# Performance work log

Measured on AMD Instinct MI355X. Metric: run time of the kernel, lower is better.

Reference implementation:

```python
import jax, jax.numpy as jnp
import numpy as np

SIZE = 256.0           # network input resolution (source: SIZE = 256)
MAX_PER_CLASS = 50     # max_output_size_per_class
MAX_TOTAL = 50         # max_total_size
IOU_THR = 0.45
SCORE_THR = 0.4


def setup_inputs() -> dict:
    key = jax.random.key(0)
    k1, k2, k3 = jax.random.split(key, 3)
    B, N, C = 64, 4032, 80
    # pixel-scale centers and sizes, as produced by the YOLO head
    xy = jax.random.uniform(k1, (B, N, 2), minval=0.0, maxval=SIZE)
    wh = jax.random.uniform(k2, (B, N, 2), minval=4.0, maxval=96.0)
    box_xywh = jnp.concatenate([xy, wh], axis=-1)
    # squared uniform -> realistic sparsity of scores above 0.4 threshold
    scores = jax.random.uniform(k3, (B, N, C)) ** 2
    return {"box_xywh": box_xywh, "scores": scores}


def _decode(box_xywh):
    # xywh (pixels) -> normalized [y1, x1, y2, x2]  (filter_boxes math)
    box_yx = box_xywh[..., 1::-1]   # (x,y) -> (y,x)
    box_hw = box_xywh[..., 3:1:-1]  # (w,h) -> (h,w)
    mins = (box_yx - box_hw * 0.5) / SIZE
    maxes = (box_yx + box_hw * 0.5) / SIZE
    return jnp.concatenate([mins, maxes], axis=-1)


def _iou_one_to_many(box, boxes):
    # box [4], boxes [N,4], yxyx format
    yx1 = jnp.maximum(box[:2], boxes[:, :2])
    yx2 = jnp.minimum(box[2:], boxes[:, 2:])
    inter = jnp.prod(jnp.clip(yx2 - yx1, 0.0), axis=-1)
    a1 = jnp.prod(jnp.clip(box[2:] - box[:2], 0.0))
    a2 = jnp.prod(jnp.clip(boxes[:, 2:] - boxes[:, :2], 0.0), axis=-1)
    return inter / (a1 + a2 - inter + 1e-9)


def _nms_single_class(boxes, scores):
    # greedy NMS for one (batch, class) lane. boxes [N,4], scores [N]
    NEG = jnp.float32(-1.0)
    s0 = jnp.where(scores >= SCORE_THR, scores, NEG)  # score filtering (filter_boxes + NMS threshold)

    def body(s, _):
        i = jnp.argmax(s)
        best = s[i]
        valid = best > 0.0
        iou = _iou_one_to_many(boxes[i], boxes)
        suppress = (iou > IOU_THR) & valid
        s = jnp.where(suppress, NEG, s).at[i].set(NEG)
        return s, (i, jnp.where(valid, best, 0.0), valid)

    _, (idx, sel, valid) = jax.lax.scan(body, s0, None, length=MAX_PER_CLASS)
    return idx, sel, valid  # each [MAX_PER_CLASS]


def _combined_nms_one_image(boxes, scores):
    # boxes [N,4] shared across classes, scores [N,C]  (combined_non_max_suppression
    # with boxes reshaped to [B,N,1,4] -> class-agnostic box coordinates)
    C = scores.shape[1]
    idx, sel, valid = jax.vmap(lambda s: _nms_single_class(boxes, s))(scores.T)  # [C,50] each
    cls_ids = jnp.broadcast_to(jnp.arange(C)[:, None], idx.shape)
    flat_scores = jnp.where(valid, sel, -1.0).reshape(-1)   # [C*50]
    top_scores, top_i = jax.lax.top_k(flat_scores, MAX_TOTAL)
    box_idx = idx.reshape(-1)[top_i]
    keep = top_scores > 0.0
    out_boxes = jnp.clip(boxes[box_idx], 0.0, 1.0)          # clip_boxes=True default
    out_boxes = jnp.where(keep[:, None], out_boxes, 0.0)
    out_scores = jnp.where(keep, top_scores, 0.0)
    out_classes = jnp.where(keep, cls_ids.reshape(-1)[top_i].astype(jnp.float32), 0.0)
    n_valid = jnp.sum(keep).astype(jnp.int32)
    return out_boxes, out_scores, out_classes, n_valid


def reference(box_xywh, scores):
    boxes = _decode(box_xywh)  # [B,N,4] normalized yxyx
    out_boxes, out_scores, out_classes, valid_detections = jax.vmap(_combined_nms_one_image)(boxes, scores)
    return out_boxes, out_scores, out_classes, valid_detections
```

## Files before the change

### kernel.cpp

```cpp
#include <hip/hip_runtime.h>
#include <cstdint>
#include <cstddef>

#pragma clang fp contract(off)

#define B_IMG 64
#define N_BOX 4032
#define C_CLS 80
#define NCH 63
#define MAX_PER_CLASS 50
#define MAX_TOTAL 50
#define FCAP 512
#define T1 0.9216f
#define T2 0.81f

__device__ __constant__ float d_flo[6] = {T1, T2, 0.6724f, 0.5476f, 0.4356f, 0.4f};

__device__ __forceinline__ float bcastf(float v, int l) {
    return __uint_as_float((unsigned)__builtin_amdgcn_readlane((int)__float_as_uint(v), l));
}
__device__ __forceinline__ unsigned long long readlane64(unsigned long long v, int l) {
    unsigned lo = (unsigned)__builtin_amdgcn_readlane((int)(unsigned)v, l);
    unsigned hi = (unsigned)__builtin_amdgcn_readlane((int)(v >> 32), l);
    return ((unsigned long long)hi << 32) | lo;
}

__device__ __forceinline__ bool iou_sup(float ay0, float ax0, float ay1, float ax1, float a1,
                                        float by0, float bx0, float by1, float bx1, float a2) {
    float y1 = fmaxf(ay0, by0), x1 = fmaxf(ax0, bx0);
    float y2 = fminf(ay1, by1), x2 = fminf(ax1, bx1);
    float inter = fmaxf(y2 - y1, 0.f) * fmaxf(x2 - x1, 0.f);
    float denom = ((a1 + a2) - inter) + 1e-9f;
    float p = 0.45f * denom;
    float diff = inter - p;
    if (__builtin_fabsf(diff) <= 2e-6f * p) return (inter / denom) > 0.45f;
    return diff > 0.f;
}

__device__ __forceinline__ int nth_set(unsigned long long m, int r) {
    int src = 0, c;
    c = __popc((unsigned)m);
    if (r >= c) { src = 32; r -= c; m >>= 32; }
    unsigned mm = (unsigned)m;
    c = __popc(mm & 0xFFFFu); if (r >= c) { src += 16; r -= c; mm >>= 16; }
    c = __popc(mm & 0xFFu);   if (r >= c) { src += 8;  r -= c; mm >>= 8; }
    c = __popc(mm & 0xFu);    if (r >= c) { src += 4;  r -= c; mm >>= 4; }
    c = __popc(mm & 0x3u);    if (r >= c) { src += 2;  r -= c; mm >>= 2; }
    c = __popc(mm & 0x1u);    if (r >= c) { src += 1; }
    return src;
}

template <int NR>
__device__ __forceinline__ void sort_buf(unsigned long long* buf, int count, int lane) {
    unsigned long long lk[NR];
    int rk[NR];
#pragma unroll
    for (int r = 0; r < NR; ++r) {
        int slot = r * 64 + lane;
        lk[r] = (slot < count) ? buf[slot] : 0ull;
        rk[r] = 0;
    }
    __builtin_amdgcn_wave_barrier();
    for (int j = 0; j < count; ++j) {
        unsigned long long kj = buf[j];
#pragma unroll
        for (int r = 0; r < NR; ++r) rk[r] += (lk[r] < kj) ? 1 : 0;
    }
    __builtin_amdgcn_wave_barrier();
#pragma unroll
    for (int r = 0; r < NR; ++r) {
        int slot = r * 64 + lane;
        if (slot < count) buf[rk[r]] = lk[r];
    }
    __builtin_amdgcn_wave_barrier();
}

__global__ __launch_bounds__(256) void fused_decode_filter(const float4* __restrict__ xywh,
                                                           const float4* __restrict__ s4,
                                                           float4* __restrict__ obox,
                                                           unsigned long long* __restrict__ bm1,
                                                           unsigned long long* __restrict__ bm2) {
    const int tid = blockIdx.x * 256 + threadIdx.x;
    const int lane = threadIdx.x & 63;
    {
        float4 v = xywh[tid];
        float hh = v.w * 0.5f, hw = v.z * 0.5f;
        float4 o;
        o.x = (v.y - hh) * (1.0f / 256.0f);
        o.y = (v.x - hw) * (1.0f / 256.0f);
        o.z = (v.y + hh) * (1.0f / 256.0f);
        o.w = (v.x + hw) * (1.0f / 256.0f);
        obox[tid] = o;
    }
    const int g = tid >> 6;
    const int b = g / NCH, h = g - b * NCH;
    const int n = h * 64 + lane;
    const float4* row = s4 + (size_t)(b * N_BOX + n) * (C_CLS / 4);
    unsigned long long w1a = 0, w2a = 0, w1b = 0, w2b = 0;
#pragma unroll
    for (int gg = 0; gg < 20; ++gg) {
        float4 v = row[gg];
        float ss[4] = {v.x, v.y, v.z, v.w};
#pragma unroll
        for (int e = 0; e < 4; ++e) {
            int c = gg * 4 + e;
            bool in1 = ss[e] >= T1;
            bool in2 = (ss[e] >= T2) && !in1;
            unsigned long long m1 = __ballot(in1);
            unsigned long long m2 = __ballot(in2);
            if (c < 64) {
                if (lane == c) { w1a = m1; w2a = m2; }
            } else {
                if (lane == c - 64) { w1b = m1; w2b = m2; }
            }
        }
    }
    size_t base = (size_t)g * C_CLS;
    bm1[base + lane] = w1a;
    bm2[base + lane] = w2a;
    if (lane < 16) {
        bm1[base + 64 + lane] = w1b;
        bm2[base + 64 + lane] = w2b;
    }
}

__global__ __launch_bounds__(256) void nms_kernel(const unsigned long long* __restrict__ bm1,
                                                  const unsigned long long* __restrict__ bm2,
                                                  const float* __restrict__ scores,
                                                  const float4* __restrict__ boxes,
                                                  float* __restrict__ cls_score,
                                                  int* __restrict__ cls_idx) {
    __shared__ unsigned long long buf_lds[4][FCAP];
    const int w = threadIdx.x >> 6, lane = threadIdx.x & 63;
    const int cl = blockIdx.x * 4 + w;
    const int b = cl / C_CLS;
    const int c = cl - b * C_CLS;
    unsigned long long* buf = buf_lds[w];
    const float4* bb = boxes + (size_t)b * N_BOX;
    const unsigned long long lmlt = (1ull << lane) - 1ull;

    float sy0 = 0.f, sx0 = 0.f, sy1 = 0.f, sx1 = 0.f, sa = 0.f;
    float my_score = -1.0f;
    int my_idx = 0;
    int n_sel = 0;

    auto process = [&](int count) {
        int pos = 0;
        while (n_sel < MAX_PER_CLASS && pos < count) {
            int blk = (count - pos < 64) ? count - pos : 64;
            unsigned long long key = (lane < blk) ? buf[pos + lane] : 0ull;
            int ci = (lane < blk) ? (int)(~(unsigned)key) : 0;
            float4 cb = bb[ci];
            if (lane >= blk) cb = make_float4(0.f, 0.f, 0.f, 0.f);
            float ca = fmaxf(cb.z - cb.x, 0.f) * fmaxf(cb.w - cb.y, 0.f);
            bool psup = false;
            for (int i = 0; i < n_sel; ++i) {
                float by0 = bcastf(sy0, i), bx0 = bcastf(sx0, i);
                float by1 = bcastf(sy1, i), bx1 = bcastf(sx1, i), ba = bcastf(sa, i);
                psup |= iou_sup(by0, bx0, by1, bx1, ba, cb.x, cb.y, cb.z, cb.w, ca);
            }
            unsigned long long supm = __ballot(psup);
            if (blk < 64) supm |= (~0ull) << blk;
            unsigned long long mjreg = 0ull;
            for (int j = 0; j < blk; ++j) {
                float jy0 = bcastf(cb.x, j), jx0 = bcastf(cb.y, j);
                float jy1 = bcastf(cb.z, j), jx1 = bcastf(cb.w, j), ja = bcastf(ca, j);
                bool sup = iou_sup(jy0, jx0, jy1, jx1, ja, cb.x, cb.y, cb.z, cb.w, ca);
                unsigned long long mj = __ballot(sup);
                if (lane == j) mjreg = mj;
            }
            unsigned long long selm = 0ull;
            int room = MAX_PER_CLASS - n_sel, taken = 0;
            for (int j = 0; j < blk; ++j) {
                if (!((supm >> j) & 1ull)) {
                    selm |= 1ull << j;
                    supm |= readlane64(mjreg, j);
                    if (++taken == room) break;
                }
            }
            int r = lane - n_sel;
            bool recv = (r >= 0) && (r < taken);
            int src = recv ? nth_set(selm, r) : 0;
            float ny0 = __shfl(cb.x, src), nx0 = __shfl(cb.y, src);
            float ny1 = __shfl(cb.z, src), nx1 = __shfl(cb.w, src);
            float na = __shfl(ca, src);
            int nsc = __shfl((int)(key >> 32), src);
            int nid = __shfl((int)(unsigned)key, src);
            if (recv) {
                sy0 = ny0; sx0 = nx0; sy1 = ny1; sx1 = nx1; sa = na;
                my_score = __uint_as_float((unsigned)nsc);
                my_idx = (int)(~(unsigned)nid);
            }
            n_sel += taken;
            pos += blk;
        }
    };

    auto load_tier = [&](const unsigned long long* bm) -> int {
        unsigned long long wd = 0ull;
        if (lane < NCH) wd = bm[(size_t)(b * NCH + lane) * C_CLS + c];
        int cntl = __popcll(wd);
        int incl = cntl;
#pragma unroll
        for (int off = 1; off < 64; off <<= 1) {
            int v = __shfl_up(incl, off);
            if (lane >= off) incl += v;
        }
        int total = __builtin_amdgcn_readlane(incl, 63);
        if (total > FCAP) return -1;
        int basep = incl - cntl;
        unsigned long long ww = wd;
        int r = 0;
        while (ww) {
            int bit = __ffsll((unsigned long long)ww) - 1;
            ww &= ww - 1;
            buf[basep + r] = (unsigned long long)(unsigned)(lane * 64 + bit);
            ++r;
        }
        __builtin_amdgcn_wave_barrier();
        const float* sp = scores + ((size_t)b * N_BOX) * C_CLS + c;
        for (int i = lane; i < total; i += 64) {
            int n = (int)buf[i];
            float s = sp[(size_t)n * C_CLS];
            buf[i] = ((unsigned long long)__float_as_uint(s) << 32) | (unsigned)(~(unsigned)n);
        }
        __builtin_amdgcn_wave_barrier();
        return total;
    };

    int dirtyStart = -1;
    {
        int cnt1 = load_tier(bm1);
        if (cnt1 < 0) dirtyStart = 0;
        else {
            if (cnt1 > 0) {
                if (cnt1 <= 256) sort_buf<4>(buf, cnt1, lane);
                else             sort_buf<8>(buf, cnt1, lane);
                process(cnt1);
            }
            if (n_sel < MAX_PER_CLASS) {
                int cnt2 = load_tier(bm2);
                if (cnt2 < 0) dirtyStart = 1;
                else {
                    if (cnt2 > 0) {
                        if (cnt2 <= 256) sort_buf<4>(buf, cnt2, lane);
                        else             sort_buf<8>(buf, cnt2, lane);
                        process(cnt2);
                    }
                    if (n_sel < MAX_PER_CLASS) dirtyStart = 2;
                }
            }
        }
    }
    for (int t = (dirtyStart < 0) ? 6 : dirtyStart; t < 6 && n_sel < MAX_PER_CLASS; ++t) {
        float lo = d_flo[t];
        float hi = (t == 0) ? 3.0e38f : d_flo[t - 1];
        const float* sp = scores + ((size_t)b * N_BOX) * C_CLS + c;
        int cnt = 0;
        for (int ch = 0; ch < N_BOX / 64; ++ch) {
            int n = ch * 64 + lane;
            float s = sp[(size_t)n * C_CLS];
            bool in = (s >= lo) && (s < hi);
            unsigned long long m = __ballot(in);
            if (in) {
                int p = cnt + (int)__popcll(m & lmlt);
                if (p < FCAP)
                    buf[p] = ((unsigned long long)__float_as_uint(s) << 32) |
                             (unsigned)(~(unsigned)n);
            }
            cnt += (int)__popcll(m);
        }
        if (cnt > FCAP) cnt = FCAP;
        if (cnt > 0) {
            sort_buf<8>(buf, cnt, lane);
            process(cnt);
        }
    }

    if (lane < MAX_PER_CLASS) {
        size_t base = (size_t)cl * MAX_PER_CLASS + lane;
        cls_score[base] = my_score;
        cls_idx[base] = my_idx;
    }
}

__global__ __launch_bounds__(256) void finalize_kernel(const float* __restrict__ cls_score,
                                                       const int* __restrict__ cls_idx,
                                                       const float4* __restrict__ boxes,
                                                       float* __restrict__ out) {
    const int b = blockIdx.x, t = threadIdx.x;
    const int lane = t & 63, wid = t >> 6;
    __shared__ unsigned long long wtop[4 * MAX_TOTAL];
    __shared__ unsigned long long res[MAX_TOTAL];
    unsigned long long k[16];
    const float* cs = cls_score + (size_t)b * (C_CLS * MAX_PER_CLASS);
#pragma unroll
    for (int j = 0; j < 16; ++j) {
        int flat = j * 256 + t;
        float s = (flat < C_CLS * MAX_PER_CLASS) ? cs[flat] : -1.0f;
        k[j] = (s > 0.0f) ? (((unsigned long long)__float_as_uint(s) << 32) |
                             (unsigned)(~(unsigned)flat))
                          : 0ull;
    }
    for (int iter = 0; iter < MAX_TOTAL; ++iter) {
        unsigned long long m = 0ull;
#pragma unroll
        for (int j = 0; j < 16; ++j)
            if (k[j] > m) m = k[j];
#pragma unroll
        for (int off = 32; off; off >>= 1) {
            unsigned long long o = __shfl_xor(m, off);
            if (o > m) m = o;
        }
        if (m == 0ull) {
            for (int r2 = iter + lane; r2 < MAX_TOTAL; r2 += 64) wtop[wid * MAX_TOTAL + r2] = 0ull;
            break;
        }
        if (lane == 0) wtop[wid * MAX_TOTAL + iter] = m;
#pragma unroll
        for (int j = 0; j < 16; ++j)
            if (k[j] == m) k[j] = 0ull;
    }
    __syncthreads();
    if (wid == 0) {
        if (lane < MAX_TOTAL) res[lane] = 0ull;
        unsigned long long lk[4];
        int rk[4];
#pragma unroll
        for (int r = 0; r < 4; ++r) {
            int slot = r * 64 + lane;
            lk[r] = (slot < 4 * MAX_TOTAL) ? wtop[slot] : 0ull;
            rk[r] = 0;
        }
        for (int j = 0; j < 4 * MAX_TOTAL; ++j) {
            unsigned long long kj = wtop[j];
#pragma unroll
            for (int r = 0; r < 4; ++r) rk[r] += (lk[r] < kj) ? 1 : 0;
        }
        __builtin_amdgcn_wave_barrier();
#pragma unroll
        for (int r = 0; r < 4; ++r)
            if (lk[r] != 0ull && rk[r] < MAX_TOTAL) res[rk[r]] = lk[r];
    }
    if (t < 64) {
        unsigned long long key = (t < MAX_TOTAL) ? res[t] : 0ull;
        bool valid = key != 0ull;
        float s = __uint_as_float((unsigned)(key >> 32));
        unsigned flat = ~(unsigned)key;
        int c = valid ? (int)(flat / 50u) : 0;
        int bidx = valid ? cls_idx[(size_t)b * (C_CLS * MAX_PER_CLASS) + flat] : 0;
        float4 bx = boxes[(size_t)b * N_BOX + bidx];
        float o0 = fminf(fmaxf(bx.x, 0.f), 1.f);
        float o1 = fminf(fmaxf(bx.y, 0.f), 1.f);
        float o2 = fminf(fmaxf(bx.z, 0.f), 1.f);
        float o3 = fminf(fmaxf(bx.w, 0.f), 1.f);
        if (t < MAX_TOTAL) {
            float* ob = out + ((size_t)b * MAX_TOTAL + t) * 4;
            ob[0] = valid ? o0 : 0.f;
            ob[1] = valid ? o1 : 0.f;
            ob[2] = valid ? o2 : 0.f;
            ob[3] = valid ? o3 : 0.f;
            out[B_IMG * MAX_TOTAL * 4 + b * MAX_TOTAL + t] = valid ? s : 0.f;
            out[B_IMG * MAX_TOTAL * 5 + b * MAX_TOTAL + t] = valid ? (float)c : 0.f;
        }
        unsigned long long vb = __ballot(valid);
        if (t == 0) out[B_IMG * MAX_TOTAL * 6 + b] = (float)__popcll(vb);
    }
}

extern "C" void kernel_launch(void* const* d_in, const int* in_sizes, int n_in,
                              void* d_out, int out_size, void* d_ws, size_t ws_size,
                              hipStream_t stream) {
    const float* xywh = (const float*)d_in[0];
    const float* scores = (const float*)d_in[1];
    float* out = (float*)d_out;
    char* ws = (char*)d_ws;

    float4* boxes_dec = (float4*)ws;
    size_t off = (size_t)B_IMG * N_BOX * 4 * sizeof(float);
    unsigned long long* bm1 = (unsigned long long*)(ws + off);
    off += (size_t)B_IMG * NCH * C_CLS * 8;
    unsigned long long* bm2 = (unsigned long long*)(ws + off);
    off += (size_t)B_IMG * NCH * C_CLS * 8;
    float* cls_score = (float*)(ws + off);
    off += (size_t)B_IMG * C_CLS * MAX_PER_CLASS * sizeof(float);
    int* cls_idx = (int*)(ws + off);

    fused_decode_filter<<<(B_IMG * N_BOX) / 256, 256, 0, stream>>>(
        (const float4*)xywh, (const float4*)scores, boxes_dec, bm1, bm2);
    nms_kernel<<<(B_IMG * C_CLS) / 4, 256, 0, stream>>>(bm1, bm2, scores, boxes_dec,
                                                        cls_score, cls_idx);
    finalize_kernel<<<B_IMG, 256, 0, stream>>>(cls_score, cls_idx, boxes_dec, out);
}
```

Baseline: 224.0 us.

## Stage scores through LDS transpose, lazy greedy NMS selection, adaptive sort size, retune tier

The filter kernel now gives each block one 64-box chunk. Its score rows are loaded coalesced into a padded LDS tile, so each wave builds bitmasks for 20 classes and fewer ballots run per thread. The NMS block loop drops the full pairwise 64x64 suppression matrix and the nth_set shuffle, and instead greedily picks the next unsuppressed candidate with ffs, computing IoU only for picked boxes. Sorting gains a 2-register variant for small buffers, and the first score tier threshold is raised so tier 1 holds fewer candidates. The greedy loop is serial per selection, and the changed tier split changes how work divides between tiers.

```diff
diff --git a/kernel.cpp b/kernel.cpp
--- a/kernel.cpp
+++ b/kernel.cpp
@@ -11,18 +11,13 @@
 #define MAX_PER_CLASS 50
 #define MAX_TOTAL 50
 #define FCAP 512
-#define T1 0.9216f
+#define T1 0.9559f
 #define T2 0.81f
 
 __device__ __constant__ float d_flo[6] = {T1, T2, 0.6724f, 0.5476f, 0.4356f, 0.4f};
 
 __device__ __forceinline__ float bcastf(float v, int l) {
     return __uint_as_float((unsigned)__builtin_amdgcn_readlane((int)__float_as_uint(v), l));
-}
-__device__ __forceinline__ unsigned long long readlane64(unsigned long long v, int l) {
-    unsigned lo = (unsigned)__builtin_amdgcn_readlane((int)(unsigned)v, l);
-    unsigned hi = (unsigned)__builtin_amdgcn_readlane((int)(v >> 32), l);
-    return ((unsigned long long)hi << 32) | lo;
 }
 
 __device__ __forceinline__ bool iou_sup(float ay0, float ax0, float ay1, float ax1, float a1,
@@ -37,19 +32,6 @@
     return diff > 0.f;
 }
 
-__device__ __forceinline__ int nth_set(unsigned long long m, int r) {
-    int src = 0, c;
-    c = __popc((unsigned)m);
-    if (r >= c) { src = 32; r -= c; m >>= 32; }
-    unsigned mm = (unsigned)m;
-    c = __popc(mm & 0xFFFFu); if (r >= c) { src += 16; r -= c; mm >>= 16; }
-    c = __popc(mm & 0xFFu);   if (r >= c) { src += 8;  r -= c; mm >>= 8; }
-    c = __popc(mm & 0xFu);    if (r >= c) { src += 4;  r -= c; mm >>= 4; }
-    c = __popc(mm & 0x3u);    if (r >= c) { src += 2;  r -= c; mm >>= 2; }
-    c = __popc(mm & 0x1u);    if (r >= c) { src += 1; }
-    return src;
-}
-
 template <int NR>
 __device__ __forceinline__ void sort_buf(unsigned long long* buf, int count, int lane) {
     unsigned long long lk[NR];
@@ -80,48 +62,45 @@
                                                            float4* __restrict__ obox,
                                                            unsigned long long* __restrict__ bm1,
                                                            unsigned long long* __restrict__ bm2) {
-    const int tid = blockIdx.x * 256 + threadIdx.x;
-    const int lane = threadIdx.x & 63;
-    {
-        float4 v = xywh[tid];
+    __shared__ float tile[64 * 81];
+    const int t = threadIdx.x;
+    const int g = blockIdx.x;
+    const int b = g / NCH, h = g - b * NCH;
+    const int boxBase = b * N_BOX + h * 64;
+    const float4* src = s4 + (size_t)boxBase * 20;
+#pragma unroll
+    for (int k = 0; k < 5; ++k) {
+        int f4 = k * 256 + t;
+        float4 v = src[f4];
+        int f = f4 * 4;
+        int n = f / 80, c = f - n * 80;
+        float* dst = tile + n * 81 + c;
+        dst[0] = v.x; dst[1] = v.y; dst[2] = v.z; dst[3] = v.w;
+    }
+    if (t < 64) {
+        float4 v = xywh[boxBase + t];
         float hh = v.w * 0.5f, hw = v.z * 0.5f;
         float4 o;
         o.x = (v.y - hh) * (1.0f / 256.0f);
         o.y = (v.x - hw) * (1.0f / 256.0f);
         o.z = (v.y + hh) * (1.0f / 256.0f);
         o.w = (v.x + hw) * (1.0f / 256.0f);
-        obox[tid] = o;
-    }
-    const int g = tid >> 6;
-    const int b = g / NCH, h = g - b * NCH;
-    const int n = h * 64 + lane;
-    const float4* row = s4 + (size_t)(b * N_BOX + n) * (C_CLS / 4);
-    unsigned long long w1a = 0, w2a = 0, w1b = 0, w2b = 0;
-#pragma unroll
-    for (int gg = 0; gg < 20; ++gg) {
-        float4 v = row[gg];
-        float ss[4] = {v.x, v.y, v.z, v.w};
-#pragma unroll
-        for (int e = 0; e < 4; ++e) {
-            int c = gg * 4 + e;
-            bool in1 = ss[e] >= T1;
-            bool in2 = (ss[e] >= T2) && !in1;
-            unsigned long long m1 = __ballot(in1);
-            unsigned long long m2 = __ballot(in2);
-            if (c < 64) {
-                if (lane == c) { w1a = m1; w2a = m2; }
-            } else {
-                if (lane == c - 64) { w1b = m1; w2b = m2; }
-            }
-        }
-    }
-    size_t base = (size_t)g * C_CLS;
-    bm1[base + lane] = w1a;
-    bm2[base + lane] = w2a;
-    if (lane < 16) {
-        bm1[base + 64 + lane] = w1b;
-        bm2[base + 64 + lane] = w2b;
-    }
+        obox[boxBase + t] = o;
+    }
+    __syncthreads();
+    const int wv = t >> 6, lane = t & 63;
+    unsigned long long w1 = 0, w2 = 0;
+    const float* col = tile + lane * 81;
+#pragma unroll
+    for (int cc = 0; cc < 20; ++cc) {
+        int c = wv * 20 + cc;
+        float s = col[c];
+        unsigned long long m1 = __ballot(s >= T1);
+        unsigned long long m2 = __ballot((s >= T2) && (s < T1));
+        if (lane == cc) { w1 = m1; w2 = m2; }
+    }
+    size_t base = (size_t)g * C_CLS + wv * 20;
+    if (lane < 20) { bm1[base + lane] = w1; bm2[base + lane] = w2; }
 }
 
 __global__ __launch_bounds__(256) void nms_kernel(const unsigned long long* __restrict__ bm1,
@@ -161,37 +140,24 @@
             }
             unsigned long long supm = __ballot(psup);
             if (blk < 64) supm |= (~0ull) << blk;
-            unsigned long long mjreg = 0ull;
-            for (int j = 0; j < blk; ++j) {
+            while (true) {
+                unsigned long long un = ~supm;
+                if (un == 0ull) break;
+                int j = __ffsll(un) - 1;
                 float jy0 = bcastf(cb.x, j), jx0 = bcastf(cb.y, j);
                 float jy1 = bcastf(cb.z, j), jx1 = bcastf(cb.w, j), ja = bcastf(ca, j);
+                int jsc = __builtin_amdgcn_readlane((int)(key >> 32), j);
+                int jid = __builtin_amdgcn_readlane((int)(unsigned)key, j);
+                if (lane == n_sel) {
+                    sy0 = jy0; sx0 = jx0; sy1 = jy1; sx1 = jx1; sa = ja;
+                    my_score = __uint_as_float((unsigned)jsc);
+                    my_idx = (int)(~(unsigned)jid);
+                }
+                if (++n_sel == MAX_PER_CLASS) break;
                 bool sup = iou_sup(jy0, jx0, jy1, jx1, ja, cb.x, cb.y, cb.z, cb.w, ca);
-                unsigned long long mj = __ballot(sup);
-                if (lane == j) mjreg = mj;
+                supm |= __ballot(sup);
+                supm |= 1ull << j;
             }
-            unsigned long long selm = 0ull;
-            int room = MAX_PER_CLASS - n_sel, taken = 0;
-            for (int j = 0; j < blk; ++j) {
-                if (!((supm >> j) & 1ull)) {
-                    selm |= 1ull << j;
-                    supm |= readlane64(mjreg, j);
-                    if (++taken == room) break;
-                }
-            }
-            int r = lane - n_sel;
-            bool recv = (r >= 0) && (r < taken);
-            int src = recv ? nth_set(selm, r) : 0;
-            float ny0 = __shfl(cb.x, src), nx0 = __shfl(cb.y, src);
-            float ny1 = __shfl(cb.z, src), nx1 = __shfl(cb.w, src);
-            float na = __shfl(ca, src);
-            int nsc = __shfl((int)(key >> 32), src);
-            int nid = __shfl((int)(unsigned)key, src);
-            if (recv) {
-                sy0 = ny0; sx0 = nx0; sy1 = ny1; sx1 = nx1; sa = na;
-                my_score = __uint_as_float((unsigned)nsc);
-                my_idx = (int)(~(unsigned)nid);
-            }
-            n_sel += taken;
             pos += blk;
         }
     };
@@ -228,25 +194,23 @@
         return total;
     };
 
+    auto sort_n = [&](int cnt) {
+        if (cnt <= 128)      sort_buf<2>(buf, cnt, lane);
+        else if (cnt <= 256) sort_buf<4>(buf, cnt, lane);
+        else                 sort_buf<8>(buf, cnt, lane);
+    };
+
     int dirtyStart = -1;
     {
         int cnt1 = load_tier(bm1);
         if (cnt1 < 0) dirtyStart = 0;
         else {
-            if (cnt1 > 0) {
-                if (cnt1 <= 256) sort_buf<4>(buf, cnt1, lane);
-                else             sort_buf<8>(buf, cnt1, lane);
-                process(cnt1);
-            }
+            if (cnt1 > 0) { sort_n(cnt1); process(cnt1); }
             if (n_sel < MAX_PER_CLASS) {
                 int cnt2 = load_tier(bm2);
                 if (cnt2 < 0) dirtyStart = 1;
                 else {
-                    if (cnt2 > 0) {
-                        if (cnt2 <= 256) sort_buf<4>(buf, cnt2, lane);
-                        else             sort_buf<8>(buf, cnt2, lane);
-                        process(cnt2);
-                    }
+                    if (cnt2 > 0) { sort_n(cnt2); process(cnt2); }
                     if (n_sel < MAX_PER_CLASS) dirtyStart = 2;
                 }
             }
@@ -271,10 +235,7 @@
             cnt += (int)__popcll(m);
         }
         if (cnt > FCAP) cnt = FCAP;
-        if (cnt > 0) {
-            sort_buf<8>(buf, cnt, lane);
-            process(cnt);
-        }
+        if (cnt > 0) { sort_n(cnt); process(cnt); }
     }
 
     if (lane < MAX_PER_CLASS) {
@@ -386,7 +347,7 @@
     off += (size_t)B_IMG * C_CLS * MAX_PER_CLASS * sizeof(float);
     int* cls_idx = (int*)(ws + off);
 
-    fused_decode_filter<<<(B_IMG * N_BOX) / 256, 256, 0, stream>>>(
+    fused_decode_filter<<<B_IMG * NCH, 256, 0, stream>>>(
         (const float4*)xywh, (const float4*)scores, boxes_dec, bm1, bm2);
     nms_kernel<<<(B_IMG * C_CLS) / 4, 256, 0, stream>>>(bm1, bm2, scores, boxes_dec,
                                                         cls_score, cls_idx);
```

New measurement: 199.1 us. -11.1%, faster.
